# Kernel tuning notes

Hardware: AMD Instinct MI355X
Metric: run time of the kernel (lower is better)

## Reference

```python
import jax, jax.numpy as jnp
import numpy as np

ALPHA = 0.8  # STE clipping threshold (unused in fwd-only path)


def binary_sign(x):
    # torch: x.sign() with zeros mapped to +1 => where(x >= 0, 1, -1)
    return jnp.where(x >= 0, jnp.ones((), x.dtype), -jnp.ones((), x.dtype))


def setup_inputs() -> dict:
    key = jax.random.key(0)
    ks = jax.random.split(key, 5)
    B, D = 16384, 4096
    x = jax.random.normal(ks[0], (B, D), dtype=jnp.float32)
    w0 = jax.random.normal(ks[1], (D, D), dtype=jnp.float32) * 0.1
    w1 = jax.random.normal(ks[2], (D, D), dtype=jnp.float32) * 0.1
    w2 = jax.random.normal(ks[3], (D, D), dtype=jnp.float32) * 0.1
    w3 = jax.random.normal(ks[4], (1, D), dtype=jnp.float32) * 0.1
    b0 = jnp.zeros((D,), jnp.float32)
    b1 = jnp.zeros((D,), jnp.float32)
    b2 = jnp.zeros((D,), jnp.float32)
    b3 = jnp.zeros((1,), jnp.float32)
    return {"x": x, "w0": w0, "b0": b0, "w1": w1, "b1": b1,
            "w2": w2, "b2": b2, "w3": w3, "b3": b3}


def reference(x, w0, b0, w1, b1, w2, b2, w3, b3):
    h = x
    for w, b in ((w0, b0), (w1, b1), (w2, b2), (w3, b3)):
        # BinaryLinear: binarize weights, dense matmul, add bias
        z = jnp.einsum('bi,oi->bo', h, binary_sign(w)) + b
        # BinaryActivation: binarize pre-activation
        h = binary_sign(z)
    return h  # [B, 1]
```

## Files before the change

kernel.cpp:

```cpp
#include <hip/hip_runtime.h>

typedef int   v4i  __attribute__((ext_vector_type(4)));
typedef int   v16i __attribute__((ext_vector_type(16)));
typedef float f4   __attribute__((ext_vector_type(4)));

#define DD 4096
#define BATCH 16384

__device__ __forceinline__ void gload16(const void* g, void* l) {
  __builtin_amdgcn_global_load_lds((const __attribute__((address_space(1))) void*)g,
                                   (__attribute__((address_space(3))) void*)l, 16, 0, 0);
}
#define ASM_VMCNT(n) asm volatile("s_waitcnt vmcnt(" #n ")" ::: "memory")
#define ASM_LGKM0()  asm volatile("s_waitcnt lgkmcnt(0)" ::: "memory")
#define BARF()       asm volatile("s_barrier" ::: "memory")

__device__ __forceinline__ int swz2(int row) { return ((row >> 1) & 3) ^ ((row >> 3) & 1); }

__global__ void binarize_swz_k(const float* __restrict__ w, unsigned char* __restrict__ o,
                               int swz_on) {
  int T = blockIdx.x * blockDim.x + threadIdx.x;
  int row = T >> 10, rem = T & 1023;
  int kblk = rem >> 4, seg = (rem >> 2) & 3, q = rem & 3;
  f4 v = *(const f4*)(w + (size_t)row * DD + kblk * 64 + seg * 16 + q * 4);
  unsigned int r = 0;
#pragma unroll
  for (int j = 0; j < 4; ++j) {
    unsigned int b = (v[j] >= 0.0f) ? 0x01u : 0xFFu;
    r |= b << (8 * j);
  }
  int slot = swz_on ? (seg ^ swz2(row)) : seg;
  *(unsigned int*)(o + (size_t)row * DD + kblk * 64 + slot * 16 + q * 4) = r;
}

__global__ void rowsum_k(const unsigned char* __restrict__ wb, int* __restrict__ R) {
  int lane = threadIdx.x & 63, wid = threadIdx.x >> 6;
  int row = blockIdx.x * 4 + wid;
  const unsigned char* p = wb + (size_t)row * DD;
  int s = 0;
#pragma unroll
  for (int j = 0; j < 4; ++j) {
    v4i a = *(const v4i*)(p + lane * 16 + j * 1024);
#pragma unroll
    for (int w = 0; w < 4; ++w) {
      unsigned int xa = (unsigned int)a[w];
#pragma unroll
      for (int by = 0; by < 4; ++by)
        s += (int)(signed char)((xa >> (8 * by)) & 255u);
    }
  }
#pragma unroll
  for (int off = 32; off > 0; off >>= 1) s += __shfl_down(s, off);
  if (lane == 0) R[row] = s;
}

__global__ void digitize_k(const float* __restrict__ x, unsigned char* __restrict__ Xd) {
  int T = blockIdx.x * blockDim.x + threadIdx.x;
  int row = T >> 10, rem = T & 1023;
  int kblk = rem >> 4, seg = (rem >> 2) & 3, q = rem & 3;
  f4 v = *(const f4*)(x + (size_t)row * DD + kblk * 64 + seg * 16 + q * 4);
  unsigned int Y[4];
#pragma unroll
  for (int j = 0; j < 4; ++j) {
    int X = (int)(v[j] * 134217728.0f);
    Y[j] = (unsigned int)(X + 1073741824);
  }
  size_t base = (size_t)row * 16384 + (size_t)kblk * 256;
  int r15 = row & 15;
#pragma unroll
  for (int d = 0; d < 4; ++d) {
    unsigned int wv = ((Y[0] >> (8 * d)) & 255u)
                    | (((Y[1] >> (8 * d)) & 255u) << 8)
                    | (((Y[2] >> (8 * d)) & 255u) << 16)
                    | (((Y[3] >> (8 * d)) & 255u) << 24);
    wv ^= 0x80808080u;
    int slot = ((d << 2) | seg) ^ r15;
    *(unsigned int*)(Xd + base + slot * 16 + q * 4) = wv;
  }
}

__global__ __launch_bounds__(256, 2) void gemm0p_k(
    const unsigned char* __restrict__ Xd, const unsigned char* __restrict__ wb,
    const int* __restrict__ R, const float* __restrict__ bias,
    signed char* __restrict__ h1) {
  __shared__ __align__(16) unsigned char As[2][64 * 256];
  __shared__ __align__(16) unsigned char Bs[2][128 * 64];
  const int tid = threadIdx.x, lane = tid & 63, wid = tid >> 6;
  const int wm = wid >> 1, wn = wid & 1;
  const int bid = blockIdx.x;
  const int xcd = bid & 7, sl = bid >> 3;
  const int m0 = ((xcd << 5) + (sl >> 5)) << 6;
  const int n0 = (sl & 31) << 7;

  v16i acc[4][2];
#pragma unroll
  for (int d = 0; d < 4; ++d)
#pragma unroll
    for (int f = 0; f < 2; ++f)
#pragma unroll
      for (int e = 0; e < 16; ++e) acc[d][f][e] = 0;

  auto stage = [&](int bf, int kb) {
#pragma unroll
    for (int i = 0; i < 4; ++i) {
      int c = wid * 4 + i;
      int lrow = c * 4 + (lane >> 4);
      const unsigned char* g = Xd + (size_t)(m0 + lrow) * 16384 + (size_t)kb * 256 + (lane & 15) * 16;
      gload16(g, &As[bf][c * 1024]);
    }
#pragma unroll
    for (int j = 0; j < 2; ++j) {
      int c = wid * 2 + j;
      int lrowB = c * 16 + (lane >> 2);
      const unsigned char* gB = wb + (size_t)(n0 + lrowB) * 4096 + kb * 64 + (lane & 3) * 16;
      gload16(gB, &Bs[bf][c * 1024]);
    }
  };

  const int rl = lane & 31, hi = lane >> 5;
  const int arow = wm * 32 + rl;
  const int r15 = arow & 15;

  stage(0, 0);
  stage(1, 1);
  ASM_VMCNT(6); BARF();
  int cur = 0;
  for (int t = 0; t < 64; ++t) {
    v4i af[2][4], bg[2][2];
#pragma unroll
    for (int kt = 0; kt < 2; ++kt) {
      int g = kt * 2 + hi;
#pragma unroll
      for (int d = 0; d < 4; ++d) {
        int slot = ((d << 2) | g) ^ r15;
        af[kt][d] = *(const v4i*)&As[cur][arow * 256 + slot * 16];
      }
#pragma unroll
      for (int f = 0; f < 2; ++f) {
        int brow = wn * 64 + f * 32 + rl;
        int slotb = g ^ swz2(brow);
        bg[kt][f] = *(const v4i*)&Bs[cur][brow * 64 + slotb * 16];
      }
    }
    __builtin_amdgcn_s_setprio(1);
#pragma unroll
    for (int d = 0; d < 4; ++d)
#pragma unroll
      for (int f = 0; f < 2; ++f)
        acc[d][f] = __builtin_amdgcn_mfma_i32_32x32x32_i8(af[0][d], bg[0][f], acc[d][f], 0, 0, 0);
    __builtin_amdgcn_s_setprio(0);
    ASM_LGKM0(); BARF();
    if (t < 62) stage(cur, t + 2);
    __builtin_amdgcn_s_setprio(1);
#pragma unroll
    for (int d = 0; d < 4; ++d)
#pragma unroll
      for (int f = 0; f < 2; ++f)
        acc[d][f] = __builtin_amdgcn_mfma_i32_32x32x32_i8(af[1][d], bg[1][f], acc[d][f], 0, 0, 0);
    __builtin_amdgcn_s_setprio(0);
    if (t < 62) { ASM_VMCNT(6); BARF(); }
    else if (t == 62) { ASM_VMCNT(0); BARF(); }
    cur ^= 1;
  }

#pragma unroll
  for (int f = 0; f < 2; ++f) {
    int col = n0 + wn * 64 + f * 32 + (lane & 31);
    long long rterm = 1082163328LL * (long long)R[col];
    double bb = (double)bias[col];
#pragma unroll
    for (int r = 0; r < 16; ++r) {
      long long Z = (long long)acc[0][f][r] + 256LL * (long long)acc[1][f][r]
                  + 65536LL * (long long)acc[2][f][r] + 16777216LL * (long long)acc[3][f][r]
                  + rterm;
      double z = (double)Z * 7.450580596923828125e-9 + bb;
      int row = m0 + wm * 32 + (r & 3) + 8 * (r >> 2) + 4 * (lane >> 5);
      int col2 = col ^ (swz2(row) << 4);
      h1[(size_t)row * DD + col2] = (z >= 0.0) ? (signed char)1 : (signed char)(-1);
    }
  }
}

__global__ __launch_bounds__(512, 2) void gemm0f_k(
    const float* __restrict__ x, const unsigned char* __restrict__ wb,
    const int* __restrict__ R, const float* __restrict__ bias,
    signed char* __restrict__ h1) {
  __shared__ signed char As[2][4][128 * 80];
  __shared__ signed char Bs[2][128 * 80];
  const int tid = threadIdx.x;
  const int lane = tid & 63, wid = tid >> 6;
  const int wm = wid >> 1, wn = wid & 1;
  const int n0 = blockIdx.x * 128, m0 = blockIdx.y * 128;

  v16i acc[4][2];
#pragma unroll
  for (int d = 0; d < 4; ++d)
#pragma unroll
    for (int f = 0; f < 2; ++f)
#pragma unroll
      for (int e = 0; e < 16; ++e) acc[d][f][e] = 0;

  const int arow_l = tid >> 4, aseg = tid & 15;
  const int brow = tid >> 2,  bseg = (tid & 3) * 16;
  f4 va[4]; v4i vb;

  auto loadTile = [&](int kpos) {
#pragma unroll
    for (int p = 0; p < 4; ++p)
      va[p] = *(const f4*)(x + (size_t)(m0 + p * 32 + arow_l) * DD + kpos + aseg * 4);
    vb = *(const v4i*)(wb + (size_t)(n0 + brow) * DD + kpos + bseg);
  };
  auto writeTile = [&](int bf) {
#pragma unroll
    for (int p = 0; p < 4; ++p) {
      int row = p * 32 + arow_l;
      unsigned int Y[4];
#pragma unroll
      for (int j = 0; j < 4; ++j) {
        int X = (int)(va[p][j] * 134217728.0f);
        Y[j] = (unsigned int)(X + 1073741824);
      }
#pragma unroll
      for (int k = 0; k < 4; ++k) {
        unsigned int wv = ((Y[0] >> (8 * k)) & 255u) | (((Y[1] >> (8 * k)) & 255u) << 8)
                        | (((Y[2] >> (8 * k)) & 255u) << 16) | (((Y[3] >> (8 * k)) & 255u) << 24);
        wv ^= 0x80808080u;
        *(unsigned int*)&As[bf][k][row * 80 + aseg * 4] = wv;
      }
    }
    *(v4i*)&Bs[bf][brow * 80 + bseg] = vb;
  };

  loadTile(0); writeTile(0);
  __syncthreads();
  for (int t = 0; t < 64; ++t) {
    int cur = t & 1;
    if (t < 63) loadTile((t + 1) * 64);
#pragma unroll
    for (int kt = 0; kt < 2; ++kt) {
      int g = kt * 2 + (lane >> 5);
      int ar = (wm * 32 + (lane & 31)) * 80 + g * 16;
      v4i a[4], b[2];
#pragma unroll
      for (int d = 0; d < 4; ++d) a[d] = *(const v4i*)&As[cur][d][ar];
#pragma unroll
      for (int f = 0; f < 2; ++f) {
        int br = wn * 64 + f * 32 + (lane & 31);
        int slotb = g ^ swz2(br);
        b[f] = *(const v4i*)&Bs[cur][br * 80 + slotb * 16];
      }
#pragma unroll
      for (int d = 0; d < 4; ++d)
#pragma unroll
        for (int f = 0; f < 2; ++f)
          acc[d][f] = __builtin_amdgcn_mfma_i32_32x32x32_i8(a[d], b[f], acc[d][f], 0, 0, 0);
    }
    if (t < 63) writeTile(cur ^ 1);
    __syncthreads();
  }

#pragma unroll
  for (int f = 0; f < 2; ++f) {
    int col = n0 + wn * 64 + f * 32 + (lane & 31);
    long long rterm = 1082163328LL * (long long)R[col];
    double bb = (double)bias[col];
#pragma unroll
    for (int r = 0; r < 16; ++r) {
      long long Z = (long long)acc[0][f][r] + 256LL * (long long)acc[1][f][r]
                  + 65536LL * (long long)acc[2][f][r] + 16777216LL * (long long)acc[3][f][r]
                  + rterm;
      double z = (double)Z * 7.450580596923828125e-9 + bb;
      int row = m0 + wm * 32 + (r & 3) + 8 * (r >> 2) + 4 * (lane >> 5);
      int col2 = col ^ (swz2(row) << 4);
      h1[(size_t)row * DD + col2] = (z >= 0.0) ? (signed char)1 : (signed char)(-1);
    }
  }
}

__global__ __launch_bounds__(256, 3) void gemm_bin_k(
    const unsigned char* __restrict__ A, const unsigned char* __restrict__ Bw,
    const float* __restrict__ bias, signed char* __restrict__ out) {
  __shared__ __align__(16) unsigned char As[2][128 * 64];
  __shared__ __align__(16) unsigned char Bs[2][128 * 64];
  const int tid = threadIdx.x, lane = tid & 63, wid = tid >> 6;
  const int wm = wid >> 1, wn = wid & 1;
  const int bid = blockIdx.x;
  const int xcd = bid & 7, sl = bid >> 3;
  const int m0 = ((xcd << 4) + (sl >> 5)) << 7;
  const int n0 = (sl & 31) << 7;

  v16i acc[2][2];
#pragma unroll
  for (int mi = 0; mi < 2; ++mi)
#pragma unroll
    for (int f = 0; f < 2; ++f)
#pragma unroll
      for (int e = 0; e < 16; ++e) acc[mi][f][e] = 0;

  auto stage = [&](int bf, int kb) {
#pragma unroll
    for (int j = 0; j < 2; ++j) {
      int c = wid * 2 + j;
      int lrow = c * 16 + (lane >> 2);
      const unsigned char* gA = A  + (size_t)(m0 + lrow) * 4096 + kb * 64 + (lane & 3) * 16;
      const unsigned char* gB = Bw + (size_t)(n0 + lrow) * 4096 + kb * 64 + (lane & 3) * 16;
      gload16(gA, &As[bf][c * 1024]);
      gload16(gB, &Bs[bf][c * 1024]);
    }
  };

  const int rl = lane & 31, hi = lane >> 5;

  stage(0, 0);
  stage(1, 1);
  ASM_VMCNT(4); BARF();
  int cur = 0;
  for (int t = 0; t < 64; ++t) {
    v4i af[2][2], bg[2][2];
#pragma unroll
    for (int kt = 0; kt < 2; ++kt) {
      int g = kt * 2 + hi;
#pragma unroll
      for (int mi = 0; mi < 2; ++mi) {
        int arow = wm * 64 + mi * 32 + rl;
        int slot = g ^ swz2(arow);
        af[kt][mi] = *(const v4i*)&As[cur][arow * 64 + slot * 16];
      }
#pragma unroll
      for (int f = 0; f < 2; ++f) {
        int brow = wn * 64 + f * 32 + rl;
        int slot = g ^ swz2(brow);
        bg[kt][f] = *(const v4i*)&Bs[cur][brow * 64 + slot * 16];
      }
    }
    __builtin_amdgcn_s_setprio(1);
#pragma unroll
    for (int mi = 0; mi < 2; ++mi)
#pragma unroll
      for (int f = 0; f < 2; ++f)
        acc[mi][f] = __builtin_amdgcn_mfma_i32_32x32x32_i8(af[0][mi], bg[0][f], acc[mi][f], 0, 0, 0);
    __builtin_amdgcn_s_setprio(0);
    ASM_LGKM0(); BARF();
    if (t < 62) stage(cur, t + 2);
    __builtin_amdgcn_s_setprio(1);
#pragma unroll
    for (int mi = 0; mi < 2; ++mi)
#pragma unroll
      for (int f = 0; f < 2; ++f)
        acc[mi][f] = __builtin_amdgcn_mfma_i32_32x32x32_i8(af[1][mi], bg[1][f], acc[mi][f], 0, 0, 0);
    __builtin_amdgcn_s_setprio(0);
    if (t < 62) { ASM_VMCNT(4); BARF(); }
    else if (t == 62) { ASM_VMCNT(0); BARF(); }
    cur ^= 1;
  }

#pragma unroll
  for (int mi = 0; mi < 2; ++mi)
#pragma unroll
    for (int f = 0; f < 2; ++f) {
      int col = n0 + wn * 64 + f * 32 + (lane & 31);
      float bb = bias[col];
#pragma unroll
      for (int r = 0; r < 16; ++r) {
        float z = (float)acc[mi][f][r] + bb;
        int row = m0 + wm * 64 + mi * 32 + (r & 3) + 8 * (r >> 2) + 4 * (lane >> 5);
        int col2 = col ^ (swz2(row) << 4);
        out[(size_t)row * DD + col2] = (z >= 0.0f) ? (signed char)1 : (signed char)(-1);
      }
    }
}

__global__ void final_k(const unsigned char* __restrict__ h, const unsigned char* __restrict__ w3b,
                        const float* __restrict__ b3, float* __restrict__ out) {
  int lane = threadIdx.x & 63, wid = threadIdx.x >> 6;
  int row = blockIdx.x * 4 + wid;
  int swz = swz2(row) << 4;
  const unsigned char* p = h + (size_t)row * DD;
  int s = 0;
#pragma unroll
  for (int j = 0; j < 4; ++j) {
    int e = lane * 16 + j * 1024;
    v4i a = *(const v4i*)(p + (e ^ swz));
    v4i b = *(const v4i*)(w3b + e);
#pragma unroll
    for (int w = 0; w < 4; ++w) {
      unsigned int xa = (unsigned int)a[w], xb = (unsigned int)b[w];
#pragma unroll
      for (int by = 0; by < 4; ++by)
        s += (int)(signed char)((xa >> (8 * by)) & 255u)
           * (int)(signed char)((xb >> (8 * by)) & 255u);
    }
  }
#pragma unroll
  for (int off = 32; off > 0; off >>= 1) s += __shfl_down(s, off);
  if (lane == 0) {
    float z = (float)s + b3[0];
    out[row] = (z >= 0.0f) ? 1.0f : -1.0f;
  }
}

extern "C" void kernel_launch(void* const* d_in, const int* in_sizes, int n_in,
                              void* d_out, int out_size, void* d_ws, size_t ws_size,
                              hipStream_t stream) {
  (void)in_sizes; (void)n_in; (void)out_size;
  const float* x  = (const float*)d_in[0];
  const float* w0 = (const float*)d_in[1];
  const float* b0 = (const float*)d_in[2];
  const float* w1 = (const float*)d_in[3];
  const float* b1 = (const float*)d_in[4];
  const float* w2 = (const float*)d_in[5];
  const float* b2 = (const float*)d_in[6];
  const float* w3 = (const float*)d_in[7];
  const float* b3 = (const float*)d_in[8];

  char* ws = (char*)d_ws;
  unsigned char* w0b = (unsigned char*)(ws + 0);
  unsigned char* w1b = (unsigned char*)(ws + (16ull << 20));
  unsigned char* w2b = (unsigned char*)(ws + (32ull << 20));
  unsigned char* w3b = (unsigned char*)(ws + (48ull << 20));
  int*           R   = (int*)(ws + (48ull << 20) + 65536);
  unsigned char* h1  = (unsigned char*)(ws + (64ull << 20));
  unsigned char* h2  = (unsigned char*)(ws + (128ull << 20));
  unsigned char* Xd  = (unsigned char*)(ws + (128ull << 20));
  float* out = (float*)d_out;

  binarize_swz_k<<<16384, 256, 0, stream>>>(w0, w0b, 1);
  binarize_swz_k<<<16384, 256, 0, stream>>>(w1, w1b, 1);
  binarize_swz_k<<<16384, 256, 0, stream>>>(w2, w2b, 1);
  binarize_swz_k<<<4,     256, 0, stream>>>(w3, w3b, 0);
  rowsum_k<<<1024, 256, 0, stream>>>(w0b, R);

  if (ws_size >= (384ull << 20)) {
    digitize_k<<<65536, 256, 0, stream>>>(x, Xd);
    gemm0p_k<<<8192, 256, 0, stream>>>(Xd, w0b, R, b0, (signed char*)h1);
  } else {
    gemm0f_k<<<dim3(32, 128), 512, 0, stream>>>(x, w0b, R, b0, (signed char*)h1);
  }
  gemm_bin_k<<<4096, 256, 0, stream>>>(h1, w1b, b1, (signed char*)h2);
  gemm_bin_k<<<4096, 256, 0, stream>>>(h2, w2b, b2, (signed char*)h1);
  final_k<<<4096, 256, 0, stream>>>(h1, w3b, b3, out);
}
```

Before: 1.974 ms.

## Software-pipeline LDS fragment reads across k-halves in both int8 GEMM kernels

Splits the per-iteration LDS fragment loads into two k-half reads. The next buffer's first half is read before the current iteration's second MFMA batch, and the second half is read before the first MFMA batch. Scheduling barriers pin the reads ahead of the MFMAs, so LDS latency can hide behind matrix work instead of stalling at the top of each iteration. In exchange, the global-load wait and barrier move to mid-iteration, ahead of the second MFMA batch. That may expose more global-load latency, and the extra live fragment registers add register pressure.

New measurement: 2.091 ms. 5.9% more time.

```diff
diff --git a/kernel.cpp b/kernel.cpp
--- a/kernel.cpp
+++ b/kernel.cpp
@@ -14,6 +14,7 @@
 #define ASM_VMCNT(n) asm volatile("s_waitcnt vmcnt(" #n ")" ::: "memory")
 #define ASM_LGKM0()  asm volatile("s_waitcnt lgkmcnt(0)" ::: "memory")
 #define BARF()       asm volatile("s_barrier" ::: "memory")
+#define SCHED0()     __builtin_amdgcn_sched_barrier(0)
 
 __device__ __forceinline__ int swz2(int row) { return ((row >> 1) & 3) ^ ((row >> 3) & 1); }
 
@@ -121,45 +122,61 @@
   const int arow = wm * 32 + rl;
   const int r15 = arow & 15;
 
+  v4i fa[4], fba[2];
+  v4i fb[4], fbb[2];
+
+  auto readKT0 = [&](int bufi) {
+    int g = 0 * 2 + hi;
+#pragma unroll
+    for (int d = 0; d < 4; ++d) {
+      int slot = ((d << 2) | g) ^ r15;
+      fa[d] = *(const v4i*)&As[bufi][arow * 256 + slot * 16];
+    }
+#pragma unroll
+    for (int f = 0; f < 2; ++f) {
+      int brow = wn * 64 + f * 32 + rl;
+      fba[f] = *(const v4i*)&Bs[bufi][brow * 64 + ((g ^ swz2(brow)) * 16)];
+    }
+  };
+  auto readKT1 = [&](int bufi) {
+    int g = 1 * 2 + hi;
+#pragma unroll
+    for (int d = 0; d < 4; ++d) {
+      int slot = ((d << 2) | g) ^ r15;
+      fb[d] = *(const v4i*)&As[bufi][arow * 256 + slot * 16];
+    }
+#pragma unroll
+    for (int f = 0; f < 2; ++f) {
+      int brow = wn * 64 + f * 32 + rl;
+      fbb[f] = *(const v4i*)&Bs[bufi][brow * 64 + ((g ^ swz2(brow)) * 16)];
+    }
+  };
+
   stage(0, 0);
   stage(1, 1);
   ASM_VMCNT(6); BARF();
+  readKT0(0);
   int cur = 0;
   for (int t = 0; t < 64; ++t) {
-    v4i af[2][4], bg[2][2];
-#pragma unroll
-    for (int kt = 0; kt < 2; ++kt) {
-      int g = kt * 2 + hi;
-#pragma unroll
-      for (int d = 0; d < 4; ++d) {
-        int slot = ((d << 2) | g) ^ r15;
-        af[kt][d] = *(const v4i*)&As[cur][arow * 256 + slot * 16];
-      }
-#pragma unroll
-      for (int f = 0; f < 2; ++f) {
-        int brow = wn * 64 + f * 32 + rl;
-        int slotb = g ^ swz2(brow);
-        bg[kt][f] = *(const v4i*)&Bs[cur][brow * 64 + slotb * 16];
-      }
-    }
+    readKT1(cur); SCHED0();
     __builtin_amdgcn_s_setprio(1);
 #pragma unroll
     for (int d = 0; d < 4; ++d)
 #pragma unroll
       for (int f = 0; f < 2; ++f)
-        acc[d][f] = __builtin_amdgcn_mfma_i32_32x32x32_i8(af[0][d], bg[0][f], acc[d][f], 0, 0, 0);
+        acc[d][f] = __builtin_amdgcn_mfma_i32_32x32x32_i8(fa[d], fba[f], acc[d][f], 0, 0, 0);
     __builtin_amdgcn_s_setprio(0);
     ASM_LGKM0(); BARF();
-    if (t < 62) stage(cur, t + 2);
+    if (t < 62) { stage(cur, t + 2); ASM_VMCNT(6); BARF(); }
+    else if (t == 62) { ASM_VMCNT(0); BARF(); }
+    if (t < 63) { readKT0(cur ^ 1); SCHED0(); }
     __builtin_amdgcn_s_setprio(1);
 #pragma unroll
     for (int d = 0; d < 4; ++d)
 #pragma unroll
       for (int f = 0; f < 2; ++f)
-        acc[d][f] = __builtin_amdgcn_mfma_i32_32x32x32_i8(af[1][d], bg[1][f], acc[d][f], 0, 0, 0);
+        acc[d][f] = __builtin_amdgcn_mfma_i32_32x32x32_i8(fb[d], fbb[f], acc[d][f], 0, 0, 0);
     __builtin_amdgcn_s_setprio(0);
-    if (t < 62) { ASM_VMCNT(6); BARF(); }
-    else if (t == 62) { ASM_VMCNT(0); BARF(); }
     cur ^= 1;
   }
 
@@ -311,46 +328,61 @@
 
   const int rl = lane & 31, hi = lane >> 5;
 
+  v4i fa[2], fba[2];
+  v4i fb[2], fbb[2];
+
+  auto readKT0 = [&](int bufi) {
+    int g = 0 * 2 + hi;
+#pragma unroll
+    for (int mi = 0; mi < 2; ++mi) {
+      int arow = wm * 64 + mi * 32 + rl;
+      fa[mi] = *(const v4i*)&As[bufi][arow * 64 + ((g ^ swz2(arow)) * 16)];
+    }
+#pragma unroll
+    for (int f = 0; f < 2; ++f) {
+      int brow = wn * 64 + f * 32 + rl;
+      fba[f] = *(const v4i*)&Bs[bufi][brow * 64 + ((g ^ swz2(brow)) * 16)];
+    }
+  };
+  auto readKT1 = [&](int bufi) {
+    int g = 1 * 2 + hi;
+#pragma unroll
+    for (int mi = 0; mi < 2; ++mi) {
+      int arow = wm * 64 + mi * 32 + rl;
+      fb[mi] = *(const v4i*)&As[bufi][arow * 64 + ((g ^ swz2(arow)) * 16)];
+    }
+#pragma unroll
+    for (int f = 0; f < 2; ++f) {
+      int brow = wn * 64 + f * 32 + rl;
+      fbb[f] = *(const v4i*)&Bs[bufi][brow * 64 + ((g ^ swz2(brow)) * 16)];
+    }
+  };
+
   stage(0, 0);
   stage(1, 1);
   ASM_VMCNT(4); BARF();
+  readKT0(0);
   int cur = 0;
   for (int t = 0; t < 64; ++t) {
-    v4i af[2][2], bg[2][2];
-#pragma unroll
-    for (int kt = 0; kt < 2; ++kt) {
-      int g = kt * 2 + hi;
-#pragma unroll
-      for (int mi = 0; mi < 2; ++mi) {
-        int arow = wm * 64 + mi * 32 + rl;
-        int slot = g ^ swz2(arow);
-        af[kt][mi] = *(const v4i*)&As[cur][arow * 64 + slot * 16];
-      }
-#pragma unroll
-      for (int f = 0; f < 2; ++f) {
-        int brow = wn * 64 + f * 32 + rl;
-        int slot = g ^ swz2(brow);
-        bg[kt][f] = *(const v4i*)&Bs[cur][brow * 64 + slot * 16];
-      }
-    }
+    readKT1(cur); SCHED0();
     __builtin_amdgcn_s_setprio(1);
 #pragma unroll
     for (int mi = 0; mi < 2; ++mi)
 #pragma unroll
       for (int f = 0; f < 2; ++f)
-        acc[mi][f] = __builtin_amdgcn_mfma_i32_32x32x32_i8(af[0][mi], bg[0][f], acc[mi][f], 0, 0, 0);
+        acc[mi][f] = __builtin_amdgcn_mfma_i32_32x32x32_i8(fa[mi], fba[f], acc[mi][f], 0, 0, 0);
     __builtin_amdgcn_s_setprio(0);
     ASM_LGKM0(); BARF();
-    if (t < 62) stage(cur, t + 2);
+    if (t < 62) { stage(cur, t + 2); ASM_VMCNT(4); BARF(); }
+    else if (t == 62) { ASM_VMCNT(0); BARF(); }
+    if (t < 63) { readKT0(cur ^ 1); SCHED0(); }
     __builtin_amdgcn_s_setprio(1);
 #pragma unroll
     for (int mi = 0; mi < 2; ++mi)
 #pragma unroll
       for (int f = 0; f < 2; ++f)
-        acc[mi][f] = __builtin_amdgcn_mfma_i32_32x32x32_i8(af[1][mi], bg[1][f], acc[mi][f], 0, 0, 0);
+        acc[mi][f] = __builtin_amdgcn_mfma_i32_32x32x32_i8(fb[mi], fbb[f], acc[mi][f], 0, 0, 0);
     __builtin_amdgcn_s_setprio(0);
-    if (t < 62) { ASM_VMCNT(4); BARF(); }
-    else if (t == 62) { ASM_VMCNT(0); BARF(); }
     cur ^= 1;
   }
 
```
